# Optimization experiments

Measured on AMD Instinct MI355X. Metric: run time of the kernel, lower is better.

Reference implementation:

```python
import jax, jax.numpy as jnp
import numpy as np

NUM_HEADS = 16
HEAD_DIM = 64  # embed_dim // num_heads
ROPE_BASE = 10000.0


def _apply_rope(x):
    # x: (B, H, S, D) -- standard rotate-half RoPE over the head dim
    B, H, S, D = x.shape
    inv_freq = 1.0 / (ROPE_BASE ** (jnp.arange(0, D, 2, dtype=jnp.float32) / D))  # (D/2,)
    ang = jnp.arange(S, dtype=jnp.float32)[:, None] * inv_freq[None, :]           # (S, D/2)
    emb = jnp.concatenate([ang, ang], axis=-1)                                     # (S, D)
    cos = jnp.cos(emb)[None, None].astype(x.dtype)
    sin = jnp.sin(emb)[None, None].astype(x.dtype)
    x1, x2 = x[..., : D // 2], x[..., D // 2 :]
    rot = jnp.concatenate([-x2, x1], axis=-1)
    return x * cos + rot * sin


def setup_inputs() -> dict:
    key = jax.random.key(0)
    ks = jax.random.split(key, 9)
    B, S, E, R = 2, 2048, 1024, 256
    s = 0.02
    return {
        "x": jax.random.normal(ks[0], (B, S, E), jnp.float32),
        "wq_down": jax.random.normal(ks[1], (R, E), jnp.float32) * s,
        "wk_rope": jax.random.normal(ks[2], (R, E), jnp.float32) * s,
        "wkv_down": jax.random.normal(ks[3], (R, E), jnp.float32) * s,
        "wq_rope": jax.random.normal(ks[4], (E, R), jnp.float32) * s,
        "wq_up": jax.random.normal(ks[5], (E, R), jnp.float32) * s,
        "wk_up": jax.random.normal(ks[6], (E, R), jnp.float32) * s,
        "wv_up": jax.random.normal(ks[7], (E, R), jnp.float32) * s,
        "wo": jax.random.normal(ks[8], (E, E), jnp.float32) * s,
    }


def _heads(t, B, S):
    # (B, S, E) -> (B, H, S, D)
    return t.reshape(B, S, NUM_HEADS, HEAD_DIM).transpose(0, 2, 1, 3)


def reference(x, wq_down, wk_rope, wkv_down, wq_rope, wq_up, wk_up, wv_up, wo):
    B, S, E = x.shape
    # low-rank query path
    q_lat = x @ wq_down.T                         # (B, S, R)
    q_r = _apply_rope(_heads(q_lat @ wq_rope.T, B, S))
    q_n = _heads(q_lat @ wq_up.T, B, S)
    q = jnp.concatenate([q_r, q_n], axis=-1)      # (B, H, S, 2D)
    # key rope path (separate latent)
    k_r = _apply_rope(_heads((x @ wk_rope.T) @ wk_up.T, B, S))
    # shared kv latent
    kv = x @ wkv_down.T                           # (B, S, R)
    k_n = _heads(kv @ wk_up.T, B, S)
    k = jnp.concatenate([k_r, k_n], axis=-1)      # (B, H, S, 2D)
    v = _heads(kv @ wv_up.T, B, S)                # (B, H, S, D)
    # causal SDPA, scale = 1/sqrt(q_dim) = 1/sqrt(2*HEAD_DIM)
    scale = 1.0 / jnp.sqrt(jnp.array(2 * HEAD_DIM, dtype=x.dtype))
    scores = jnp.einsum("bhqd,bhkd->bhqk", q, k) * scale
    mask = jnp.tril(jnp.ones((S, S), dtype=bool))
    scores = jnp.where(mask[None, None], scores, jnp.finfo(scores.dtype).min)
    attn = jax.nn.softmax(scores, axis=-1)
    y = jnp.einsum("bhqk,bhkd->bhqd", attn, v)    # (B, H, S, D)
    y = y.transpose(0, 2, 1, 3).reshape(B, S, E)
    return y @ wo.T
```

## Files before the change

### kernel.cpp

```cpp
#include <hip/hip_runtime.h>
#include <hip/hip_bf16.h>
#include <math.h>


typedef __attribute__((ext_vector_type(8))) short  short8;
typedef __attribute__((ext_vector_type(4))) float  floatx4;

static __device__ __forceinline__ unsigned short f2bf(float f) {
    __hip_bfloat16 h = __float2bfloat16(f);
    return *reinterpret_cast<unsigned short*>(&h);
}

#define GLL16(gp, lp) __builtin_amdgcn_global_load_lds( \
    (const __attribute__((address_space(1))) void*)(gp), \
    (__attribute__((address_space(3))) void*)(lp), 16, 0, 0)

struct CastDesc { const float* src; unsigned short* dst; int n4; };
struct CastArgs { CastDesc d[8]; };

__global__ __launch_bounds__(256) void cast_bf16_multi(CastArgs a)
{
    CastDesc dd = a.d[blockIdx.y];
    const int stride = gridDim.x * 256;
    for (int i = blockIdx.x * 256 + threadIdx.x; i < dd.n4; i += stride) {
        float4 v = ((const float4*)dd.src)[i];
        ushort4 o = make_ushort4(f2bf(v.x), f2bf(v.y), f2bf(v.z), f2bf(v.w));
        ((ushort4*)dd.dst)[i] = o;
    }
}

template<int MODE, bool CVTA>
__global__ __launch_bounds__(128) void gemm64(
    const void* __restrict__ Ain, int lda,
    const unsigned short* __restrict__ B0,
    const unsigned short* __restrict__ B1,
    const unsigned short* __restrict__ B2, int nspan, int ldb,
    void* __restrict__ Cout, int ldc, int K, float oscale)
{
    __shared__ __align__(16) unsigned short As[64 * 32];
    __shared__ __align__(16) unsigned short Bs[64 * 32];

    const int t    = threadIdx.x;
    const int w    = t >> 6;
    const int lane = t & 63;
    const int li   = lane & 15;
    const int quad = lane >> 4;
    const int m0   = blockIdx.y * 64;
    const int n0   = blockIdx.x * 64;

    const unsigned short* Bp = (n0 < nspan) ? B0 : ((n0 < 2 * nspan) ? B1 : B2);
    const int nb0 = n0 % nspan;

    const int arow = m0 + w * 32 + (lane >> 2);
    const int acg  = (lane & 3) * 8;
    const int acs  = (((lane & 3) ^ ((lane >> 3) & 3))) * 8;
    const int cq   = (quad ^ ((li >> 1) & 3)) * 8;
    const unsigned short* gb = Bp + (size_t)(nb0 + w * 32 + (lane >> 2)) * ldb + acs;
    unsigned short* lA0 = &As[(w * 32) * 32];
    unsigned short* lA1 = &As[(w * 32 + 16) * 32];
    unsigned short* lB0 = &Bs[(w * 32) * 32];
    unsigned short* lB1 = &Bs[(w * 32 + 16) * 32];
    unsigned short* wA0 = &As[(w * 32 + (lane >> 2)) * 32 + acs];
    unsigned short* wA1 = wA0 + 16 * 32;

    floatx4 acc[2][4];
    #pragma unroll
    for (int i = 0; i < 2; ++i)
        #pragma unroll
        for (int j = 0; j < 4; ++j)
            acc[i][j] = (floatx4){0.f, 0.f, 0.f, 0.f};

    for (int k0 = 0; k0 < K; k0 += 32) {
        if (CVTA) {
            const float* Af = (const float*)Ain;
            const float* ga0 = Af + (size_t)arow * lda + k0 + acg;
            float4 a00 = *(const float4*)(ga0);
            float4 a01 = *(const float4*)(ga0 + 4);
            float4 a10 = *(const float4*)(ga0 + (size_t)16 * lda);
            float4 a11 = *(const float4*)(ga0 + (size_t)16 * lda + 4);
            __syncthreads();
            GLL16(gb + k0,            lB0);
            GLL16(gb + 16 * ldb + k0, lB1);
            ushort4 p0 = make_ushort4(f2bf(a00.x), f2bf(a00.y), f2bf(a00.z), f2bf(a00.w));
            ushort4 p1 = make_ushort4(f2bf(a01.x), f2bf(a01.y), f2bf(a01.z), f2bf(a01.w));
            ushort4 p2 = make_ushort4(f2bf(a10.x), f2bf(a10.y), f2bf(a10.z), f2bf(a10.w));
            ushort4 p3 = make_ushort4(f2bf(a11.x), f2bf(a11.y), f2bf(a11.z), f2bf(a11.w));
            *(ushort4*)(wA0)     = p0;
            *(ushort4*)(wA0 + 4) = p1;
            *(ushort4*)(wA1)     = p2;
            *(ushort4*)(wA1 + 4) = p3;
            __syncthreads();
        } else {
            const unsigned short* Ab = (const unsigned short*)Ain;
            const unsigned short* ga = Ab + (size_t)arow * lda + acs;
            __syncthreads();
            GLL16(ga + k0,            lA0);
            GLL16(ga + 16 * lda + k0, lA1);
            GLL16(gb + k0,            lB0);
            GLL16(gb + 16 * ldb + k0, lB1);
            __syncthreads();
        }

        short8 af[2], bfr[4];
        #pragma unroll
        for (int mb = 0; mb < 2; ++mb)
            af[mb] = *(const short8*)&As[(w * 32 + mb * 16 + li) * 32 + cq];
        #pragma unroll
        for (int nb = 0; nb < 4; ++nb)
            bfr[nb] = *(const short8*)&Bs[(nb * 16 + li) * 32 + cq];
        #pragma unroll
        for (int mb = 0; mb < 2; ++mb)
            #pragma unroll
            for (int nb = 0; nb < 4; ++nb)
                acc[mb][nb] = __builtin_amdgcn_mfma_f32_16x16x32_bf16(
                    af[mb], bfr[nb], acc[mb][nb], 0, 0, 0);
    }

    if (MODE == 0) {
        float* C = (float*)Cout;
        #pragma unroll
        for (int mb = 0; mb < 2; ++mb)
            #pragma unroll
            for (int nb = 0; nb < 4; ++nb) {
                const int m = m0 + w * 32 + mb * 16 + quad * 4;
                const int n = n0 + nb * 16 + li;
                #pragma unroll
                for (int r = 0; r < 4; ++r)
                    C[(size_t)(m + r) * ldc + n] = acc[mb][nb][r] * oscale;
            }
    } else {
        unsigned short* C = (unsigned short*)Cout;
        #pragma unroll
        for (int mb = 0; mb < 2; ++mb)
            #pragma unroll
            for (int nb = 0; nb < 4; ++nb) {
                const int m = m0 + w * 32 + mb * 16 + quad * 4;
                const int n = n0 + nb * 16 + li;
                #pragma unroll
                for (int r = 0; r < 4; ++r)
                    C[(size_t)(m + r) * ldc + n] = f2bf(acc[mb][nb][r] * oscale);
            }
    }
}

__global__ __launch_bounds__(256) void gemm_qkv(
    const unsigned short* __restrict__ lat,
    const unsigned short* __restrict__ wqr, const unsigned short* __restrict__ wqu,
    const unsigned short* __restrict__ wku, const unsigned short* __restrict__ wvu,
    unsigned short* __restrict__ Qp, unsigned short* __restrict__ Kp,
    unsigned short* __restrict__ Vt, float qscale)
{
    __shared__ __align__(16) unsigned short As[128 * 32];
    __shared__ __align__(16) unsigned short Bs[128 * 32];

    const int t    = threadIdx.x;
    const int w    = t >> 6;
    const int lane = t & 63;
    const int li   = lane & 15;
    const int quad = lane >> 4;
    const int wr   = w >> 1, wc = w & 1;
    const int m0   = blockIdx.y * 128;
    const int n0   = blockIdx.x * 128;

    const unsigned short* Ap;
    const unsigned short* Bp;
    int nloc, seg;
    if (n0 < 1024)      { seg = 0; Ap = lat;       Bp = wqr; nloc = n0; }
    else if (n0 < 2048) { seg = 1; Ap = lat;       Bp = wqu; nloc = n0 - 1024; }
    else if (n0 < 3072) { seg = 2; Ap = lat + 256; Bp = wku; nloc = n0 - 2048; }
    else if (n0 < 4096) { seg = 3; Ap = lat + 512; Bp = wku; nloc = n0 - 3072; }
    else                { seg = 4; Ap = lat + 512; Bp = wvu; nloc = n0 - 4096; }
    const float oscale = (seg <= 1) ? qscale : 1.0f;

    const int acs = (((lane & 3) ^ ((lane >> 3) & 3))) * 8;
    const int cq  = (quad ^ ((li >> 1) & 3)) * 8;
    const unsigned short* ga = Ap + (size_t)(m0   + w * 32 + (lane >> 2)) * 768 + acs;
    const unsigned short* gb = Bp + (size_t)(nloc + w * 32 + (lane >> 2)) * 256 + acs;
    unsigned short* lA0 = &As[(w * 32) * 32];
    unsigned short* lA1 = &As[(w * 32 + 16) * 32];
    unsigned short* lB0 = &Bs[(w * 32) * 32];
    unsigned short* lB1 = &Bs[(w * 32 + 16) * 32];

    floatx4 acc[4][4];
    #pragma unroll
    for (int i = 0; i < 4; ++i)
        #pragma unroll
        for (int j = 0; j < 4; ++j)
            acc[i][j] = (floatx4){0.f, 0.f, 0.f, 0.f};

    for (int k0 = 0; k0 < 256; k0 += 32) {
        __syncthreads();
        GLL16(ga + k0,            lA0);
        GLL16(ga + 16 * 768 + k0, lA1);
        GLL16(gb + k0,            lB0);
        GLL16(gb + 16 * 256 + k0, lB1);
        __syncthreads();

        short8 af[4], bfr[4];
        #pragma unroll
        for (int mb = 0; mb < 4; ++mb)
            af[mb] = *(const short8*)&As[(wr * 64 + mb * 16 + li) * 32 + cq];
        #pragma unroll
        for (int nb = 0; nb < 4; ++nb)
            bfr[nb] = *(const short8*)&Bs[(wc * 64 + nb * 16 + li) * 32 + cq];
        #pragma unroll
        for (int mb = 0; mb < 4; ++mb)
            #pragma unroll
            for (int nb = 0; nb < 4; ++nb)
                acc[mb][nb] = __builtin_amdgcn_mfma_f32_16x16x32_bf16(
                    af[mb], bfr[nb], acc[mb][nb], 0, 0, 0);
    }

    const int h = ((nloc + wc * 64) >> 6) & 15;

    if (seg == 0) {
        float invf[2];
        #pragma unroll
        for (int nb = 0; nb < 2; ++nb)
            invf[nb] = exp2f((float)(nb * 16 + li) * -0.4152410118609203f);
        #pragma unroll
        for (int mb = 0; mb < 4; ++mb) {
            const int m = m0 + wr * 64 + mb * 16 + quad * 4;
            const int b = m >> 11, s = m & 2047;
            #pragma unroll
            for (int nb = 0; nb < 2; ++nb) {
                const int dd = nb * 16 + li;
                size_t o = ((size_t)(b * 16 + h) * 2048 + s) * 128 + dd;
                #pragma unroll
                for (int r = 0; r < 4; ++r) {
                    float ang = (float)(s + r) * invf[nb];
                    float sn, cs;
                    __sincosf(ang, &sn, &cs);
                    float x1 = acc[mb][nb][r], x2 = acc[mb][nb + 2][r];
                    Qp[o + (size_t)r * 128]      = f2bf((x1 * cs - x2 * sn) * oscale);
                    Qp[o + (size_t)r * 128 + 32] = f2bf((x2 * cs + x1 * sn) * oscale);
                }
            }
        }
    } else if (seg == 1) {
        #pragma unroll
        for (int mb = 0; mb < 4; ++mb)
            #pragma unroll
            for (int nb = 0; nb < 4; ++nb) {
                const int m = m0 + wr * 64 + mb * 16 + quad * 4;
                const int n = nloc + wc * 64 + nb * 16 + li;
                const int dn = n & 63;
                const int b = m >> 11, s = m & 2047;
                size_t o = ((size_t)(b * 16 + h) * 2048 + s) * 128 + 64 + dn;
                #pragma unroll
                for (int r = 0; r < 4; ++r)
                    Qp[o + (size_t)r * 128] = f2bf(acc[mb][nb][r] * oscale);
            }
    } else if (seg == 2) {
        float invf[2];
        #pragma unroll
        for (int nb = 0; nb < 2; ++nb)
            invf[nb] = exp2f((float)(nb * 16 + li) * -0.4152410118609203f);
        #pragma unroll
        for (int mb = 0; mb < 4; ++mb) {
            const int m = m0 + wr * 64 + mb * 16 + quad * 4;
            const int b = m >> 11, sba = m & 2047;
            #pragma unroll
            for (int nb = 0; nb < 2; ++nb) {
                const int dd = nb * 16 + li;
                const int d2 = dd + 32;
                #pragma unroll
                for (int r = 0; r < 4; ++r) {
                    const int s = sba + r;
                    float ang = (float)s * invf[nb];
                    float sn, cs;
                    __sincosf(ang, &sn, &cs);
                    float x1 = acc[mb][nb][r], x2 = acc[mb][nb + 2][r];
                    size_t base = (size_t)(b * 16 + h) * 262144
                                + (size_t)(s >> 5) * 4096 + (size_t)(s & 31) * 8;
                    Kp[base + (dd >> 3) * 256 + (dd & 7)] = f2bf(x1 * cs - x2 * sn);
                    Kp[base + (d2 >> 3) * 256 + (d2 & 7)] = f2bf(x2 * cs + x1 * sn);
                }
            }
        }
    } else if (seg == 3) {
        #pragma unroll
        for (int mb = 0; mb < 4; ++mb)
            #pragma unroll
            for (int nb = 0; nb < 4; ++nb) {
                const int m = m0 + wr * 64 + mb * 16 + quad * 4;
                const int n = nloc + wc * 64 + nb * 16 + li;
                const int d = 64 + (n & 63);
                const int b = m >> 11, sba = m & 2047;
                #pragma unroll
                for (int r = 0; r < 4; ++r) {
                    const int s = sba + r;
                    size_t o = (size_t)(b * 16 + h) * 262144 + (size_t)(s >> 5) * 4096
                             + (size_t)(d >> 3) * 256 + (size_t)(s & 31) * 8 + (d & 7);
                    Kp[o] = f2bf(acc[mb][nb][r]);
                }
            }
    } else {
        #pragma unroll
        for (int mb = 0; mb < 4; ++mb)
            #pragma unroll
            for (int nb = 0; nb < 4; ++nb) {
                const int m = m0 + wr * 64 + mb * 16 + quad * 4;
                const int n = nloc + wc * 64 + nb * 16 + li;
                const int dn = n & 63;
                const int b = m >> 11, s = m & 2047;
                ushort4 st = make_ushort4(f2bf(acc[mb][nb][0]), f2bf(acc[mb][nb][1]),
                                          f2bf(acc[mb][nb][2]), f2bf(acc[mb][nb][3]));
                size_t o = (size_t)(b * 16 + h) * 131072 + (size_t)(s >> 5) * 2048
                         + (size_t)((s & 31) >> 3) * 512 + (size_t)dn * 8 + (s & 7);
                *(ushort4*)&Vt[o] = st;
            }
    }
}

__global__ __launch_bounds__(256, 4) void attn_mfma(
    const unsigned short* __restrict__ Qp, const unsigned short* __restrict__ Kp,
    const unsigned short* __restrict__ Vt, unsigned short* __restrict__ y,
    float* __restrict__ O0, float* __restrict__ O1,
    float* __restrict__ l0, float* __restrict__ l1)
{
    __shared__ __align__(16) unsigned short Ks[2][4096];
    __shared__ __align__(16) unsigned short PT[4][640];

    const int t    = threadIdx.x;
    const int w    = t >> 6;
    const int lane = t & 63;
    const int li   = lane & 15;
    const int quad = lane >> 4;

    const int blk = blockIdx.x;
    const int xcd = blk & 7;
    const int g   = blk >> 3;
    const int bh  = xcd + 8 * (g & 3);
    const int u   = g >> 2;
    const int p   = u >> 1;
    const int var = u & 1;
    const int b   = bh >> 4, h = bh & 15;

    const unsigned short* Kb = Kp + (size_t)bh * 262144;
    const unsigned short* Vb = Vt + (size_t)bh * 131072;

    short8 onesf;
    #pragma unroll
    for (int j = 0; j < 8; ++j) onesf[j] = (short)0x3F80;

    unsigned short* Pw = &PT[w][0];

    auto run_seg = [&](int qt, int lo, int hi, int mode) {
        const int qbase  = qt * 64 + w * 16;
        const int lastkt = 2 * qt + (w >> 1);

        const unsigned short* Qb = Qp + ((size_t)bh * 2048 + qbase) * 128;
        short8 qf[4];
        #pragma unroll
        for (int kb = 0; kb < 4; ++kb)
            qf[kb] = *(const short8*)(Qb + (size_t)li * 128 + kb * 32 + quad * 8);

        floatx4 o0 = {0.f,0.f,0.f,0.f}, o1 = {0.f,0.f,0.f,0.f};
        floatx4 o2 = {0.f,0.f,0.f,0.f}, o3 = {0.f,0.f,0.f,0.f};
        floatx4 ol = {0.f,0.f,0.f,0.f};

        auto stageK = [&](int kt, int buf) {
            const unsigned short* gk = Kb + (size_t)kt * 4096 + w * 1024 + (size_t)lane * 8;
            GLL16(gk,       &Ks[buf][w * 1024]);
            GLL16(gk + 512, &Ks[buf][w * 1024 + 512]);
        };
        auto loadV = [&](int kt, short8 vf[4]) {
            const unsigned short* gv = Vb + (size_t)kt * 2048 + quad * 512 + li * 8;
            #pragma unroll
            for (int nb = 0; nb < 4; ++nb)
                vf[nb] = *(const short8*)(gv + nb * 128);
        };
        auto compute = [&](int kt, int buf, short8 vf[4], bool maskTile) {
            const int kbase = kt * 32;
            floatx4 s0 = {0.f,0.f,0.f,0.f}, s1 = {0.f,0.f,0.f,0.f};
            #pragma unroll
            for (int kb = 0; kb < 4; ++kb) {
                short8 k0 = *(const short8*)&Ks[buf][(kb * 4 + quad) * 256 + li * 8];
                short8 k1 = *(const short8*)&Ks[buf][(kb * 4 + quad) * 256 + (16 + li) * 8];
                s0 = __builtin_amdgcn_mfma_f32_16x16x32_bf16(qf[kb], k0, s0, 0, 0, 0);
                s1 = __builtin_amdgcn_mfma_f32_16x16x32_bf16(qf[kb], k1, s1, 0, 0, 0);
            }
            #pragma unroll
            for (int r = 0; r < 4; ++r) {
                const int i = quad * 4 + r;
                unsigned int u0 = __float_as_uint(__expf(s0[r])) >> 16;
                unsigned int u1 = __float_as_uint(__expf(s1[r])) >> 16;
                if (maskTile) {
                    const int qrow = qbase + i;
                    u0 = (kbase + li      <= qrow) ? u0 : 0u;
                    u1 = (kbase + 16 + li <= qrow) ? u1 : 0u;
                }
                Pw[i * 40 + li]      = (unsigned short)u0;
                Pw[i * 40 + 16 + li] = (unsigned short)u1;
            }
            short8 pf = *(const short8*)&Pw[li * 40 + quad * 8];

            ol = __builtin_amdgcn_mfma_f32_16x16x32_bf16(pf, onesf, ol, 0, 0, 0);
            o0 = __builtin_amdgcn_mfma_f32_16x16x32_bf16(pf, vf[0], o0, 0, 0, 0);
            o1 = __builtin_amdgcn_mfma_f32_16x16x32_bf16(pf, vf[1], o1, 0, 0, 0);
            o2 = __builtin_amdgcn_mfma_f32_16x16x32_bf16(pf, vf[2], o2, 0, 0, 0);
            o3 = __builtin_amdgcn_mfma_f32_16x16x32_bf16(pf, vf[3], o3, 0, 0, 0);
        };

        short8 vfa[4], vfb[4];
        __syncthreads();
        stageK(lo, 0);
        if (lo <= lastkt) loadV(lo, vfa);

        int kt = lo;
        while (true) {
            __syncthreads();
            if (kt + 1 < hi) {
                stageK(kt + 1, 1);
                if (kt + 1 <= lastkt) loadV(kt + 1, vfb);
            }
            if (kt <= lastkt) compute(kt, 0, vfa, kt == lastkt);
            ++kt; if (kt == hi) break;
            __syncthreads();
            if (kt + 1 < hi) {
                stageK(kt + 1, 0);
                if (kt + 1 <= lastkt) loadV(kt + 1, vfa);
            }
            if (kt <= lastkt) compute(kt, 1, vfb, kt == lastkt);
            ++kt; if (kt == hi) break;
        }

        if (mode == 0) {
            unsigned short* yb2 = y + ((size_t)b * 2048 + qbase + quad * 4) * 1024 + h * 64 + li;
            #pragma unroll
            for (int r = 0; r < 4; ++r) {
                const float linv = 1.0f / ol[r];
                yb2[(size_t)r * 1024 + 0]  = f2bf(o0[r] * linv);
                yb2[(size_t)r * 1024 + 16] = f2bf(o1[r] * linv);
                yb2[(size_t)r * 1024 + 32] = f2bf(o2[r] * linv);
                yb2[(size_t)r * 1024 + 48] = f2bf(o3[r] * linv);
            }
        } else {
            float* Op = (mode == 1) ? O0 : O1;
            float* lp = (mode == 1) ? l0 : l1;
            const int rowL = qbase - 1024 + quad * 4;
            float* ob = Op + ((size_t)bh * 1024 + rowL) * 64 + li;
            #pragma unroll
            for (int r = 0; r < 4; ++r) {
                ob[(size_t)r * 64 + 0]  = o0[r];
                ob[(size_t)r * 64 + 16] = o1[r];
                ob[(size_t)r * 64 + 32] = o2[r];
                ob[(size_t)r * 64 + 48] = o3[r];
            }
            if (li == 0) {
                #pragma unroll
                for (int r = 0; r < 4; ++r)
                    lp[bh * 1024 + rowL + r] = ol[r];
            }
        }
    };

    if (var == 0) {
        run_seg(p, 0, 2 * p + 2, 0);
        run_seg(31 - p, 0, 31 - 2 * p, 1);
    } else {
        run_seg(31 - p, 31 - 2 * p, 64 - 2 * p, 2);
    }
}

__global__ __launch_bounds__(256) void attn_combine(
    const float* __restrict__ O0, const float* __restrict__ O1,
    const float* __restrict__ l0, const float* __restrict__ l1,
    unsigned short* __restrict__ y)
{
    const int idx = blockIdx.x * 256 + threadIdx.x;
    const int c4  = idx & 15;
    const int row = (idx >> 4) & 1023;
    const int bh  = idx >> 14;
    const int b   = bh >> 4, h = bh & 15;

    const size_t o = ((size_t)bh * 1024 + row) * 64 + c4 * 4;
    float4 a  = *(const float4*)&O0[o];
    float4 c  = *(const float4*)&O1[o];
    const float linv = 1.0f / (l0[bh * 1024 + row] + l1[bh * 1024 + row]);

    ushort4 st = make_ushort4(f2bf((a.x + c.x) * linv), f2bf((a.y + c.y) * linv),
                              f2bf((a.z + c.z) * linv), f2bf((a.w + c.w) * linv));
    const size_t yo = ((size_t)b * 2048 + 1024 + row) * 1024 + h * 64 + c4 * 4;
    *(ushort4*)&y[yo] = st;
}

extern "C" void kernel_launch(void* const* d_in, const int* in_sizes, int n_in,
                              void* d_out, int out_size, void* d_ws, size_t ws_size,
                              hipStream_t stream)
{
    const float* x        = (const float*)d_in[0];
    const float* wq_down  = (const float*)d_in[1];
    const float* wk_rope  = (const float*)d_in[2];
    const float* wkv_down = (const float*)d_in[3];
    const float* wq_rope  = (const float*)d_in[4];
    const float* wq_up    = (const float*)d_in[5];
    const float* wk_up    = (const float*)d_in[6];
    const float* wv_up    = (const float*)d_in[7];
    const float* wo       = (const float*)d_in[8];
    float* out = (float*)d_out;

    char* wsb = (char*)d_ws;
    const size_t MB = 1u << 20;
    unsigned short* lat  = (unsigned short*)(wsb + 8 * MB);
    unsigned short* Qp   = (unsigned short*)(wsb + 14 * MB);
    unsigned short* Kp   = (unsigned short*)(wsb + 30 * MB);
    unsigned short* Vt   = (unsigned short*)(wsb + 46 * MB);
    unsigned short* yb   = (unsigned short*)(wsb + 54 * MB);
    unsigned short* wqd_b = (unsigned short*)(wsb + 62 * MB);
    unsigned short* wkr_b = (unsigned short*)(wsb + 63 * MB);
    unsigned short* wkd_b = (unsigned short*)(wsb + 64 * MB);
    unsigned short* wqr_b = (unsigned short*)(wsb + 65 * MB);
    unsigned short* wqu_b = (unsigned short*)(wsb + 66 * MB);
    unsigned short* wku_b = (unsigned short*)(wsb + 67 * MB);
    unsigned short* wvu_b = (unsigned short*)(wsb + 68 * MB);
    unsigned short* wo_b  = (unsigned short*)(wsb + 69 * MB);
    float* O0p = (float*)(wsb + 71 * MB);
    float* O1p = (float*)(wsb + 79 * MB);
    float* l0p = (float*)(wsb + 87 * MB);
    float* l1p = (float*)(wsb + 87 * MB + (1u << 17));

    const float scale = 0.08838834764831845f;
    const int BIG = 1 << 30;
    dim3 blk(256);

    CastArgs ca;
    ca.d[0] = { wq_down,  wqd_b,  262144 / 4 };
    ca.d[1] = { wk_rope,  wkr_b,  262144 / 4 };
    ca.d[2] = { wkv_down, wkd_b,  262144 / 4 };
    ca.d[3] = { wq_rope,  wqr_b,  262144 / 4 };
    ca.d[4] = { wq_up,    wqu_b,  262144 / 4 };
    ca.d[5] = { wk_up,    wku_b,  262144 / 4 };
    ca.d[6] = { wv_up,    wvu_b,  262144 / 4 };
    ca.d[7] = { wo,       wo_b,  1048576 / 4 };
    cast_bf16_multi<<<dim3(64, 8), blk, 0, stream>>>(ca);

    gemm64<3, true><<<dim3(12, 64), dim3(128), 0, stream>>>(
        x, 1024, wqd_b, wkr_b, wkd_b, 256, 1024, lat, 768, 1024, 1.f);

    gemm_qkv<<<dim3(40, 32), blk, 0, stream>>>(
        lat, wqr_b, wqu_b, wku_b, wvu_b, Qp, Kp, Vt, scale);

    attn_mfma<<<dim3(1024), blk, 0, stream>>>(Qp, Kp, Vt, yb, O0p, O1p, l0p, l1p);
    attn_combine<<<dim3(2048), blk, 0, stream>>>(O0p, O1p, l0p, l1p, yb);

    gemm64<0, false><<<dim3(16, 64), dim3(128), 0, stream>>>(
        yb, 1024, wo_b, wo_b, wo_b, BIG, 1024, out, 1024, 1024, 1.f);
}
```

Measured before the change: 210.8 us.

## Keep attention probabilities in registers by transposing the QK MFMA

```diff
diff --git a/kernel.cpp b/kernel.cpp
--- a/kernel.cpp
+++ b/kernel.cpp
@@ -4,6 +4,7 @@
 
 
 typedef __attribute__((ext_vector_type(8))) short  short8;
+typedef __attribute__((ext_vector_type(4))) short  short4b;
 typedef __attribute__((ext_vector_type(4))) float  floatx4;
 
 static __device__ __forceinline__ unsigned short f2bf(float f) {
@@ -320,7 +321,6 @@
     float* __restrict__ l0, float* __restrict__ l1)
 {
     __shared__ __align__(16) unsigned short Ks[2][4096];
-    __shared__ __align__(16) unsigned short PT[4][640];
 
     const int t    = threadIdx.x;
     const int w    = t >> 6;
@@ -344,8 +344,6 @@
     #pragma unroll
     for (int j = 0; j < 8; ++j) onesf[j] = (short)0x3F80;
 
-    unsigned short* Pw = &PT[w][0];
-
     auto run_seg = [&](int qt, int lo, int hi, int mode) {
         const int qbase  = qt * 64 + w * 16;
         const int lastkt = 2 * qt + (w >> 1);
@@ -366,10 +364,17 @@
             GLL16(gk + 512, &Ks[buf][w * 1024 + 512]);
         };
         auto loadV = [&](int kt, short8 vf[4]) {
-            const unsigned short* gv = Vb + (size_t)kt * 2048 + quad * 512 + li * 8;
-            #pragma unroll
-            for (int nb = 0; nb < 4; ++nb)
-                vf[nb] = *(const short8*)(gv + nb * 128);
+            const unsigned short* gv = Vb + (size_t)kt * 2048
+                                     + (quad >> 1) * 512 + (quad & 1) * 4 + li * 8;
+            #pragma unroll
+            for (int nb = 0; nb < 4; ++nb) {
+                short4b vlo = *(const short4b*)(gv + nb * 128);
+                short4b vhi = *(const short4b*)(gv + nb * 128 + 1024);
+                short8 v;
+                v[0] = vlo[0]; v[1] = vlo[1]; v[2] = vlo[2]; v[3] = vlo[3];
+                v[4] = vhi[0]; v[5] = vhi[1]; v[6] = vhi[2]; v[7] = vhi[3];
+                vf[nb] = v;
+            }
         };
         auto compute = [&](int kt, int buf, short8 vf[4], bool maskTile) {
             const int kbase = kt * 32;
@@ -378,24 +383,22 @@
             for (int kb = 0; kb < 4; ++kb) {
                 short8 k0 = *(const short8*)&Ks[buf][(kb * 4 + quad) * 256 + li * 8];
                 short8 k1 = *(const short8*)&Ks[buf][(kb * 4 + quad) * 256 + (16 + li) * 8];
-                s0 = __builtin_amdgcn_mfma_f32_16x16x32_bf16(qf[kb], k0, s0, 0, 0, 0);
-                s1 = __builtin_amdgcn_mfma_f32_16x16x32_bf16(qf[kb], k1, s1, 0, 0, 0);
-            }
+                s0 = __builtin_amdgcn_mfma_f32_16x16x32_bf16(k0, qf[kb], s0, 0, 0, 0);
+                s1 = __builtin_amdgcn_mfma_f32_16x16x32_bf16(k1, qf[kb], s1, 0, 0, 0);
+            }
+            short8 pf;
+            const int qrow = qbase + li;
             #pragma unroll
             for (int r = 0; r < 4; ++r) {
-                const int i = quad * 4 + r;
                 unsigned int u0 = __float_as_uint(__expf(s0[r])) >> 16;
                 unsigned int u1 = __float_as_uint(__expf(s1[r])) >> 16;
                 if (maskTile) {
-                    const int qrow = qbase + i;
-                    u0 = (kbase + li      <= qrow) ? u0 : 0u;
-                    u1 = (kbase + 16 + li <= qrow) ? u1 : 0u;
+                    u0 = (kbase + quad * 4 + r      <= qrow) ? u0 : 0u;
+                    u1 = (kbase + 16 + quad * 4 + r <= qrow) ? u1 : 0u;
                 }
-                Pw[i * 40 + li]      = (unsigned short)u0;
-                Pw[i * 40 + 16 + li] = (unsigned short)u1;
-            }
-            short8 pf = *(const short8*)&Pw[li * 40 + quad * 8];
-
+                pf[r]     = (short)u0;
+                pf[4 + r] = (short)u1;
+            }
             ol = __builtin_amdgcn_mfma_f32_16x16x32_bf16(pf, onesf, ol, 0, 0, 0);
             o0 = __builtin_amdgcn_mfma_f32_16x16x32_bf16(pf, vf[0], o0, 0, 0, 0);
             o1 = __builtin_amdgcn_mfma_f32_16x16x32_bf16(pf, vf[1], o1, 0, 0, 0);
```

Measured after the change: 220.7 us. 4.7% more time.

## Fuse weight casts and attention split-combine into consuming GEMM loads

Applied to the files above, without the earlier changes.

```diff
diff --git a/kernel.cpp b/kernel.cpp
--- a/kernel.cpp
+++ b/kernel.cpp
@@ -15,26 +15,13 @@
     (const __attribute__((address_space(1))) void*)(gp), \
     (__attribute__((address_space(3))) void*)(lp), 16, 0, 0)
 
-struct CastDesc { const float* src; unsigned short* dst; int n4; };
-struct CastArgs { CastDesc d[8]; };
-
-__global__ __launch_bounds__(256) void cast_bf16_multi(CastArgs a)
-{
-    CastDesc dd = a.d[blockIdx.y];
-    const int stride = gridDim.x * 256;
-    for (int i = blockIdx.x * 256 + threadIdx.x; i < dd.n4; i += stride) {
-        float4 v = ((const float4*)dd.src)[i];
-        ushort4 o = make_ushort4(f2bf(v.x), f2bf(v.y), f2bf(v.z), f2bf(v.w));
-        ((ushort4*)dd.dst)[i] = o;
-    }
-}
-
-template<int MODE, bool CVTA>
+template<int MODE, bool CVTA, bool CVTB, bool COMB>
 __global__ __launch_bounds__(128) void gemm64(
     const void* __restrict__ Ain, int lda,
-    const unsigned short* __restrict__ B0,
-    const unsigned short* __restrict__ B1,
-    const unsigned short* __restrict__ B2, int nspan, int ldb,
+    const void* __restrict__ B0v, const void* __restrict__ B1v,
+    const void* __restrict__ B2v, int nspan, int ldb,
+    const float* __restrict__ Oa, const float* __restrict__ Ob,
+    const float* __restrict__ la, const float* __restrict__ lb,
     void* __restrict__ Cout, int ldc, int K, float oscale)
 {
     __shared__ __align__(16) unsigned short As[64 * 32];
@@ -48,20 +35,27 @@
     const int m0   = blockIdx.y * 64;
     const int n0   = blockIdx.x * 64;
 
-    const unsigned short* Bp = (n0 < nspan) ? B0 : ((n0 < 2 * nspan) ? B1 : B2);
+    const int bsel = (n0 < nspan) ? 0 : ((n0 < 2 * nspan) ? 1 : 2);
+    const void* Bv = (bsel == 0) ? B0v : ((bsel == 1) ? B1v : B2v);
     const int nb0 = n0 % nspan;
 
     const int arow = m0 + w * 32 + (lane >> 2);
+    const int brow = nb0 + w * 32 + (lane >> 2);
     const int acg  = (lane & 3) * 8;
     const int acs  = (((lane & 3) ^ ((lane >> 3) & 3))) * 8;
     const int cq   = (quad ^ ((li >> 1) & 3)) * 8;
-    const unsigned short* gb = Bp + (size_t)(nb0 + w * 32 + (lane >> 2)) * ldb + acs;
     unsigned short* lA0 = &As[(w * 32) * 32];
     unsigned short* lA1 = &As[(w * 32 + 16) * 32];
     unsigned short* lB0 = &Bs[(w * 32) * 32];
     unsigned short* lB1 = &Bs[(w * 32 + 16) * 32];
     unsigned short* wA0 = &As[(w * 32 + (lane >> 2)) * 32 + acs];
     unsigned short* wA1 = wA0 + 16 * 32;
+    unsigned short* wB0 = &Bs[(w * 32 + (lane >> 2)) * 32 + acs];
+    unsigned short* wB1 = wB0 + 16 * 32;
+
+    const bool upper = COMB && ((m0 & 2047) >= 1024);
+    const int rowL = (arow & 2047) - 1024;
+    const int bb   = arow >> 11;
 
     floatx4 acc[2][4];
     #pragma unroll
@@ -71,35 +65,81 @@
             acc[i][j] = (floatx4){0.f, 0.f, 0.f, 0.f};
 
     for (int k0 = 0; k0 < K; k0 += 32) {
+        float4 a00, a01, a10, a11;
+        float4 p00, p01, p10, p11, q00, q01, q10, q11;
+        float lv0 = 0.f, lv1 = 0.f;
         if (CVTA) {
             const float* Af = (const float*)Ain;
             const float* ga0 = Af + (size_t)arow * lda + k0 + acg;
-            float4 a00 = *(const float4*)(ga0);
-            float4 a01 = *(const float4*)(ga0 + 4);
-            float4 a10 = *(const float4*)(ga0 + (size_t)16 * lda);
-            float4 a11 = *(const float4*)(ga0 + (size_t)16 * lda + 4);
-            __syncthreads();
+            a00 = *(const float4*)(ga0);
+            a01 = *(const float4*)(ga0 + 4);
+            a10 = *(const float4*)(ga0 + (size_t)16 * lda);
+            a11 = *(const float4*)(ga0 + (size_t)16 * lda + 4);
+        }
+        if (COMB && upper) {
+            const int nc = k0 + acg;
+            const int hh = nc >> 6, d0 = nc & 63;
+            const size_t ob0 = ((size_t)((bb * 16 + hh) * 1024 + rowL)) * 64 + d0;
+            const size_t ob1 = ob0 + (size_t)16 * 64;
+            p00 = *(const float4*)(Oa + ob0);
+            p01 = *(const float4*)(Oa + ob0 + 4);
+            q00 = *(const float4*)(Ob + ob0);
+            q01 = *(const float4*)(Ob + ob0 + 4);
+            p10 = *(const float4*)(Oa + ob1);
+            p11 = *(const float4*)(Oa + ob1 + 4);
+            q10 = *(const float4*)(Ob + ob1);
+            q11 = *(const float4*)(Ob + ob1 + 4);
+            const int lbase = (bb * 16 + hh) * 1024 + rowL;
+            lv0 = 1.0f / (la[lbase] + lb[lbase]);
+            lv1 = 1.0f / (la[lbase + 16] + lb[lbase + 16]);
+        }
+        float4 b00, b01, b10, b11;
+        if (CVTB) {
+            const float* Bf = (const float*)Bv;
+            const float* gb0 = Bf + (size_t)brow * ldb + k0 + acg;
+            b00 = *(const float4*)(gb0);
+            b01 = *(const float4*)(gb0 + 4);
+            b10 = *(const float4*)(gb0 + (size_t)16 * ldb);
+            b11 = *(const float4*)(gb0 + (size_t)16 * ldb + 4);
+        }
+
+        __syncthreads();
+
+        if (!CVTA && !(COMB && upper)) {
+            const unsigned short* Ab = (const unsigned short*)Ain;
+            const unsigned short* ga = Ab + (size_t)arow * lda + acs;
+            GLL16(ga + k0,            lA0);
+            GLL16(ga + 16 * lda + k0, lA1);
+        }
+        if (!CVTB) {
+            const unsigned short* Bb = (const unsigned short*)Bv;
+            const unsigned short* gb = Bb + (size_t)brow * ldb + acs;
             GLL16(gb + k0,            lB0);
             GLL16(gb + 16 * ldb + k0, lB1);
-            ushort4 p0 = make_ushort4(f2bf(a00.x), f2bf(a00.y), f2bf(a00.z), f2bf(a00.w));
-            ushort4 p1 = make_ushort4(f2bf(a01.x), f2bf(a01.y), f2bf(a01.z), f2bf(a01.w));
-            ushort4 p2 = make_ushort4(f2bf(a10.x), f2bf(a10.y), f2bf(a10.z), f2bf(a10.w));
-            ushort4 p3 = make_ushort4(f2bf(a11.x), f2bf(a11.y), f2bf(a11.z), f2bf(a11.w));
-            *(ushort4*)(wA0)     = p0;
-            *(ushort4*)(wA0 + 4) = p1;
-            *(ushort4*)(wA1)     = p2;
-            *(ushort4*)(wA1 + 4) = p3;
-            __syncthreads();
-        } else {
-            const unsigned short* Ab = (const unsigned short*)Ain;
-            const unsigned short* ga = Ab + (size_t)arow * lda + acs;
-            __syncthreads();
-            GLL16(ga + k0,            lA0);
-            GLL16(ga + 16 * lda + k0, lA1);
-            GLL16(gb + k0,            lB0);
-            GLL16(gb + 16 * ldb + k0, lB1);
-            __syncthreads();
-        }
+        }
+        if (CVTA) {
+            *(ushort4*)(wA0)     = make_ushort4(f2bf(a00.x), f2bf(a00.y), f2bf(a00.z), f2bf(a00.w));
+            *(ushort4*)(wA0 + 4) = make_ushort4(f2bf(a01.x), f2bf(a01.y), f2bf(a01.z), f2bf(a01.w));
+            *(ushort4*)(wA1)     = make_ushort4(f2bf(a10.x), f2bf(a10.y), f2bf(a10.z), f2bf(a10.w));
+            *(ushort4*)(wA1 + 4) = make_ushort4(f2bf(a11.x), f2bf(a11.y), f2bf(a11.z), f2bf(a11.w));
+        }
+        if (COMB && upper) {
+            *(ushort4*)(wA0)     = make_ushort4(f2bf((p00.x + q00.x) * lv0), f2bf((p00.y + q00.y) * lv0),
+                                                f2bf((p00.z + q00.z) * lv0), f2bf((p00.w + q00.w) * lv0));
+            *(ushort4*)(wA0 + 4) = make_ushort4(f2bf((p01.x + q01.x) * lv0), f2bf((p01.y + q01.y) * lv0),
+                                                f2bf((p01.z + q01.z) * lv0), f2bf((p01.w + q01.w) * lv0));
+            *(ushort4*)(wA1)     = make_ushort4(f2bf((p10.x + q10.x) * lv1), f2bf((p10.y + q10.y) * lv1),
+                                                f2bf((p10.z + q10.z) * lv1), f2bf((p10.w + q10.w) * lv1));
+            *(ushort4*)(wA1 + 4) = make_ushort4(f2bf((p11.x + q11.x) * lv1), f2bf((p11.y + q11.y) * lv1),
+                                                f2bf((p11.z + q11.z) * lv1), f2bf((p11.w + q11.w) * lv1));
+        }
+        if (CVTB) {
+            *(ushort4*)(wB0)     = make_ushort4(f2bf(b00.x), f2bf(b00.y), f2bf(b00.z), f2bf(b00.w));
+            *(ushort4*)(wB0 + 4) = make_ushort4(f2bf(b01.x), f2bf(b01.y), f2bf(b01.z), f2bf(b01.w));
+            *(ushort4*)(wB1)     = make_ushort4(f2bf(b10.x), f2bf(b10.y), f2bf(b10.z), f2bf(b10.w));
+            *(ushort4*)(wB1 + 4) = make_ushort4(f2bf(b11.x), f2bf(b11.y), f2bf(b11.z), f2bf(b11.w));
+        }
+        __syncthreads();
 
         short8 af[2], bfr[4];
         #pragma unroll
@@ -145,8 +185,8 @@
 
 __global__ __launch_bounds__(256) void gemm_qkv(
     const unsigned short* __restrict__ lat,
-    const unsigned short* __restrict__ wqr, const unsigned short* __restrict__ wqu,
-    const unsigned short* __restrict__ wku, const unsigned short* __restrict__ wvu,
+    const float* __restrict__ wqr, const float* __restrict__ wqu,
+    const float* __restrict__ wku, const float* __restrict__ wvu,
     unsigned short* __restrict__ Qp, unsigned short* __restrict__ Kp,
     unsigned short* __restrict__ Vt, float qscale)
 {
@@ -163,7 +203,7 @@
     const int n0   = blockIdx.x * 128;
 
     const unsigned short* Ap;
-    const unsigned short* Bp;
+    const float* Bp;
     int nloc, seg;
     if (n0 < 1024)      { seg = 0; Ap = lat;       Bp = wqr; nloc = n0; }
     else if (n0 < 2048) { seg = 1; Ap = lat;       Bp = wqu; nloc = n0 - 1024; }
@@ -172,14 +212,15 @@
     else                { seg = 4; Ap = lat + 512; Bp = wvu; nloc = n0 - 4096; }
     const float oscale = (seg <= 1) ? qscale : 1.0f;
 
+    const int acg = (lane & 3) * 8;
     const int acs = (((lane & 3) ^ ((lane >> 3) & 3))) * 8;
     const int cq  = (quad ^ ((li >> 1) & 3)) * 8;
-    const unsigned short* ga = Ap + (size_t)(m0   + w * 32 + (lane >> 2)) * 768 + acs;
-    const unsigned short* gb = Bp + (size_t)(nloc + w * 32 + (lane >> 2)) * 256 + acs;
+    const unsigned short* ga = Ap + (size_t)(m0 + w * 32 + (lane >> 2)) * 768 + acs;
+    const float* gbf = Bp + (size_t)(nloc + w * 32 + (lane >> 2)) * 256 + acg;
     unsigned short* lA0 = &As[(w * 32) * 32];
     unsigned short* lA1 = &As[(w * 32 + 16) * 32];
-    unsigned short* lB0 = &Bs[(w * 32) * 32];
-    unsigned short* lB1 = &Bs[(w * 32 + 16) * 32];
+    unsigned short* wB0 = &Bs[(w * 32 + (lane >> 2)) * 32 + acs];
+    unsigned short* wB1 = wB0 + 16 * 32;
 
     floatx4 acc[4][4];
     #pragma unroll
@@ -189,11 +230,17 @@
             acc[i][j] = (floatx4){0.f, 0.f, 0.f, 0.f};
 
     for (int k0 = 0; k0 < 256; k0 += 32) {
+        float4 b00 = *(const float4*)(gbf + k0);
+        float4 b01 = *(const float4*)(gbf + k0 + 4);
+        float4 b10 = *(const float4*)(gbf + (size_t)16 * 256 + k0);
+        float4 b11 = *(const float4*)(gbf + (size_t)16 * 256 + k0 + 4);
         __syncthreads();
         GLL16(ga + k0,            lA0);
         GLL16(ga + 16 * 768 + k0, lA1);
-        GLL16(gb + k0,            lB0);
-        GLL16(gb + 16 * 256 + k0, lB1);
+        *(ushort4*)(wB0)     = make_ushort4(f2bf(b00.x), f2bf(b00.y), f2bf(b00.z), f2bf(b00.w));
+        *(ushort4*)(wB0 + 4) = make_ushort4(f2bf(b01.x), f2bf(b01.y), f2bf(b01.z), f2bf(b01.w));
+        *(ushort4*)(wB1)     = make_ushort4(f2bf(b10.x), f2bf(b10.y), f2bf(b10.z), f2bf(b10.w));
+        *(ushort4*)(wB1 + 4) = make_ushort4(f2bf(b11.x), f2bf(b11.y), f2bf(b11.z), f2bf(b11.w));
         __syncthreads();
 
         short8 af[4], bfr[4];
@@ -462,28 +509,6 @@
     } else {
         run_seg(31 - p, 31 - 2 * p, 64 - 2 * p, 2);
     }
-}
-
-__global__ __launch_bounds__(256) void attn_combine(
-    const float* __restrict__ O0, const float* __restrict__ O1,
-    const float* __restrict__ l0, const float* __restrict__ l1,
-    unsigned short* __restrict__ y)
-{
-    const int idx = blockIdx.x * 256 + threadIdx.x;
-    const int c4  = idx & 15;
-    const int row = (idx >> 4) & 1023;
-    const int bh  = idx >> 14;
-    const int b   = bh >> 4, h = bh & 15;
-
-    const size_t o = ((size_t)bh * 1024 + row) * 64 + c4 * 4;
-    float4 a  = *(const float4*)&O0[o];
-    float4 c  = *(const float4*)&O1[o];
-    const float linv = 1.0f / (l0[bh * 1024 + row] + l1[bh * 1024 + row]);
-
-    ushort4 st = make_ushort4(f2bf((a.x + c.x) * linv), f2bf((a.y + c.y) * linv),
-                              f2bf((a.z + c.z) * linv), f2bf((a.w + c.w) * linv));
-    const size_t yo = ((size_t)b * 2048 + 1024 + row) * 1024 + h * 64 + c4 * 4;
-    *(ushort4*)&y[yo] = st;
 }
 
 extern "C" void kernel_launch(void* const* d_in, const int* in_sizes, int n_in,
@@ -508,43 +533,24 @@
     unsigned short* Kp   = (unsigned short*)(wsb + 30 * MB);
     unsigned short* Vt   = (unsigned short*)(wsb + 46 * MB);
     unsigned short* yb   = (unsigned short*)(wsb + 54 * MB);
-    unsigned short* wqd_b = (unsigned short*)(wsb + 62 * MB);
-    unsigned short* wkr_b = (unsigned short*)(wsb + 63 * MB);
-    unsigned short* wkd_b = (unsigned short*)(wsb + 64 * MB);
-    unsigned short* wqr_b = (unsigned short*)(wsb + 65 * MB);
-    unsigned short* wqu_b = (unsigned short*)(wsb + 66 * MB);
-    unsigned short* wku_b = (unsigned short*)(wsb + 67 * MB);
-    unsigned short* wvu_b = (unsigned short*)(wsb + 68 * MB);
-    unsigned short* wo_b  = (unsigned short*)(wsb + 69 * MB);
-    float* O0p = (float*)(wsb + 71 * MB);
-    float* O1p = (float*)(wsb + 79 * MB);
-    float* l0p = (float*)(wsb + 87 * MB);
-    float* l1p = (float*)(wsb + 87 * MB + (1u << 17));
+    float* O0p = (float*)(wsb + 62 * MB);
+    float* O1p = (float*)(wsb + 70 * MB);
+    float* l0p = (float*)(wsb + 78 * MB);
+    float* l1p = (float*)(wsb + 78 * MB + (1u << 17));
 
     const float scale = 0.08838834764831845f;
     const int BIG = 1 << 30;
-    dim3 blk(256);
-
-    CastArgs ca;
-    ca.d[0] = { wq_down,  wqd_b,  262144 / 4 };
-    ca.d[1] = { wk_rope,  wkr_b,  262144 / 4 };
-    ca.d[2] = { wkv_down, wkd_b,  262144 / 4 };
-    ca.d[3] = { wq_rope,  wqr_b,  262144 / 4 };
-    ca.d[4] = { wq_up,    wqu_b,  262144 / 4 };
-    ca.d[5] = { wk_up,    wku_b,  262144 / 4 };
-    ca.d[6] = { wv_up,    wvu_b,  262144 / 4 };
-    ca.d[7] = { wo,       wo_b,  1048576 / 4 };
-    cast_bf16_multi<<<dim3(64, 8), blk, 0, stream>>>(ca);
-
-    gemm64<3, true><<<dim3(12, 64), dim3(128), 0, stream>>>(
-        x, 1024, wqd_b, wkr_b, wkd_b, 256, 1024, lat, 768, 1024, 1.f);
-
-    gemm_qkv<<<dim3(40, 32), blk, 0, stream>>>(
-        lat, wqr_b, wqu_b, wku_b, wvu_b, Qp, Kp, Vt, scale);
-
-    attn_mfma<<<dim3(1024), blk, 0, stream>>>(Qp, Kp, Vt, yb, O0p, O1p, l0p, l1p);
-    attn_combine<<<dim3(2048), blk, 0, stream>>>(O0p, O1p, l0p, l1p, yb);
-
-    gemm64<0, false><<<dim3(16, 64), dim3(128), 0, stream>>>(
-        yb, 1024, wo_b, wo_b, wo_b, BIG, 1024, out, 1024, 1024, 1.f);
+
+    gemm64<3, true, true, false><<<dim3(12, 64), dim3(128), 0, stream>>>(
+        x, 1024, wq_down, wk_rope, wkv_down, 256, 1024,
+        nullptr, nullptr, nullptr, nullptr, lat, 768, 1024, 1.f);
+
+    gemm_qkv<<<dim3(40, 32), dim3(256), 0, stream>>>(
+        lat, wq_rope, wq_up, wk_up, wv_up, Qp, Kp, Vt, scale);
+
+    attn_mfma<<<dim3(1024), dim3(256), 0, stream>>>(Qp, Kp, Vt, yb, O0p, O1p, l0p, l1p);
+
+    gemm64<0, false, true, true><<<dim3(16, 64), dim3(128), 0, stream>>>(
+        yb, 1024, wo, wo, wo, BIG, 1024,
+        O0p, O1p, l0p, l1p, out, 1024, 1024, 1.f);
 }
```

Result: slower. 223.7 us (+6.1%).
